# Kernel tuning notes

Hardware: AMD Instinct MI355X
Metric: run time of the kernel (lower is better)

The kernel has to match this reference:

```python
import jax, jax.numpy as jnp
import numpy as np

N = 50000
HID = 128
NH = 4
E_RES, E_SEQ, E_KNN = 100000, 100000, 200000
BN_EPS = 1e-5
NEG_SLOPE = 0.2


def _gat(h, src, dst, W, al, ar, resW, b):
    """DGL-style GATConv (eval mode: feat_drop off, residual=True, bias).
    h: (N, in), W/resW: (in, H*out), al/ar: (H, out), b: (H*out,)"""
    Hh, out = al.shape
    feat = (h @ W).reshape(N, Hh, out)                 # (N, H, out)
    el = jnp.sum(feat * al, axis=-1)                   # (N, H)
    er = jnp.sum(feat * ar, axis=-1)                   # (N, H)
    e = jax.nn.leaky_relu(el[src] + er[dst], NEG_SLOPE)  # (E, H)
    # edge softmax over incoming edges of each dst node (numerically stable)
    m = jax.ops.segment_max(e, dst, num_segments=N)    # (N, H)
    ex = jnp.exp(e - m[dst])
    s = jax.ops.segment_sum(ex, dst, num_segments=N)
    a = ex / s[dst]                                    # (E, H)
    msg = a[:, :, None] * feat[src]                    # (E, H, out)
    rst = jax.ops.segment_sum(msg, dst, num_segments=N)  # (N, H, out)
    return rst + (h @ resW).reshape(N, Hh, out) + b.reshape(1, Hh, out)


def _hetero(h, src_res, dst_res, src_seq, dst_seq, src_knn, dst_knn, W, al, ar, resW, b):
    # HeteroGraphConv with aggregate='sum' over relations, then mean over heads
    r = _gat(h, src_res, dst_res, W[0], al[0], ar[0], resW[0], b[0])
    r = r + _gat(h, src_seq, dst_seq, W[1], al[1], ar[1], resW[1], b[1])
    r = r + _gat(h, src_knn, dst_knn, W[2], al[2], ar[2], resW[2], b[2])
    return jnp.mean(r, axis=1)                         # (N, out)


def setup_inputs() -> dict:
    key = jax.random.key(0)
    ks = iter(jax.random.split(key, 32))
    inp = {}
    inp["x"] = jax.random.normal(next(ks), (N, HID), jnp.float32)
    inp["src_res"] = jax.random.randint(next(ks), (E_RES,), 0, N, jnp.int32)
    inp["dst_res"] = jax.random.randint(next(ks), (E_RES,), 0, N, jnp.int32)
    inp["src_seq"] = jax.random.randint(next(ks), (E_SEQ,), 0, N, jnp.int32)
    inp["dst_seq"] = jax.random.randint(next(ks), (E_SEQ,), 0, N, jnp.int32)
    inp["src_knn"] = jax.random.randint(next(ks), (E_KNN,), 0, N, jnp.int32)
    inp["dst_knn"] = jax.random.randint(next(ks), (E_KNN,), 0, N, jnp.int32)
    sc = 0.05
    for l in (0, 1):
        inp[f"W{l}"] = jax.random.normal(next(ks), (3, HID, NH * HID), jnp.float32) * sc
        inp[f"al{l}"] = jax.random.normal(next(ks), (3, NH, HID), jnp.float32) * sc
        inp[f"ar{l}"] = jax.random.normal(next(ks), (3, NH, HID), jnp.float32) * sc
        inp[f"resW{l}"] = jax.random.normal(next(ks), (3, HID, NH * HID), jnp.float32) * sc
        inp[f"b{l}"] = jax.random.normal(next(ks), (3, NH * HID), jnp.float32) * sc
    inp["fc_W"] = jax.random.normal(next(ks), (HID, HID), jnp.float32) * sc
    inp["fc_b"] = jax.random.normal(next(ks), (HID,), jnp.float32) * sc
    inp["bn_gamma"] = jnp.ones((HID,), jnp.float32)
    inp["bn_beta"] = jnp.zeros((HID,), jnp.float32)
    inp["bn_mean"] = jax.random.normal(next(ks), (HID,), jnp.float32) * sc
    inp["bn_var"] = jax.random.uniform(next(ks), (HID,), jnp.float32)
    return inp


def reference(x, src_res, dst_res, src_seq, dst_seq, src_knn, dst_knn,
              W0, al0, ar0, resW0, b0, W1, al1, ar1, resW1, b1,
              fc_W, fc_b, bn_gamma, bn_beta, bn_mean, bn_var):
    # layer 0: hetero GAT, head-mean, fc + ReLU + BatchNorm (eval), dropout=identity
    h = _hetero(x, src_res, dst_res, src_seq, dst_seq, src_knn, dst_knn,
                W0, al0, ar0, resW0, b0)
    h = jax.nn.relu(h @ fc_W + fc_b)
    h = (h - bn_mean) / jnp.sqrt(bn_var + BN_EPS) * bn_gamma + bn_beta
    # layer 1 (final): hetero GAT, head-mean
    out = _hetero(h, src_res, dst_res, src_seq, dst_seq, src_knn, dst_knn,
                  W1, al1, ar1, resW1, b1)
    return out
```

## Files before the change

### kernel.cpp

```cpp
#include <hip/hip_runtime.h>
#include <hip/hip_bf16.h>
#include <math.h>
#include <stdint.h>

#define NNODES 50000
#define SCHUNK 4096
#define AW 1664
#define XOFF 1536

typedef __bf16 bf16x8 __attribute__((ext_vector_type(8)));
typedef float f32x4 __attribute__((ext_vector_type(4)));
typedef unsigned short u16;
typedef unsigned int u32;

__device__ __forceinline__ float lrelu(float x){ return x >= 0.f ? x : 0.2f*x; }
__device__ __forceinline__ float lo2f(u32 v){ union{ u32 i; float f; } c; c.i = v<<16; return c.f; }
__device__ __forceinline__ float hi2f(u32 v){ union{ u32 i; float f; } c; c.i = v & 0xffff0000u; return c.f; }
__device__ __forceinline__ u16 f2b(float f){ __hip_bfloat16 h = __float2bfloat16(f); return *(u16*)&h; }
__device__ __forceinline__ u32 packbf(float a, float b){ return (u32)f2b(a) | ((u32)f2b(b) << 16); }

#define GLDS16(g, l) __builtin_amdgcn_global_load_lds( \
    (const __attribute__((address_space(1))) void*)(g), \
    (__attribute__((address_space(3))) void*)(l), 16, 0, 0)

__global__ void prep_all(const float* __restrict__ W0, const float* __restrict__ W1,
                         const float* __restrict__ resW0, const float* __restrict__ resW1,
                         const float* __restrict__ b0, const float* __restrict__ b1,
                         const float* __restrict__ al0, const float* __restrict__ ar0,
                         const float* __restrict__ al1, const float* __restrict__ ar1,
                         const float* __restrict__ fcW,
                         u16* __restrict__ Btb, float* __restrict__ biasf,
                         u16* __restrict__ wlb, u16* __restrict__ fcWtb,
                         int* __restrict__ cnt)
{
    int gid = blockIdx.x*blockDim.x + threadIdx.x;
    if (gid < 3*NNODES) cnt[gid] = 0;
    if (gid < 2*128*AW){
        int l = gid / (128*AW);
        int rem = gid - l*(128*AW);
        int c = rem / AW;
        int j = rem - c*AW;
        const float* W  = l ? W1 : W0;
        const float* rw = l ? resW1 : resW0;
        float v;
        if (j < XOFF){
            int r = j >> 9, h = (j >> 7) & 3, k = j & 127;
            v = 0.25f * W[(size_t)r*65536 + (size_t)k*512 + h*128 + c];
        } else {
            int k = j - XOFF;
            float s = 0.f;
            for (int r = 0; r < 3; ++r)
                for (int h = 0; h < 4; ++h)
                    s += rw[(size_t)r*65536 + (size_t)k*512 + h*128 + c];
            v = 0.25f * s;
        }
        Btb[gid] = f2b(v);
    }
    if (gid < 256){
        int l = gid >> 7, c = gid & 127;
        const float* bb = l ? b1 : b0;
        float s = 0.f;
        for (int r = 0; r < 3; ++r)
            for (int h = 0; h < 4; ++h)
                s += bb[r*512 + h*128 + c];
        biasf[gid] = 0.25f*s;
    }
    if (gid < 2*128*128){
        int l = gid >> 14;
        int col = (gid >> 7) & 127;
        int k = gid & 127;
        float v = 0.f;
        if (col < 24){
            int r = col >> 3, lr = (col >> 2) & 1, h = col & 3;
            const float* W = l ? W1 : W0;
            const float* av = l ? (lr ? ar1 : al1) : (lr ? ar0 : al0);
            const float* wrow = W + (size_t)r*65536 + (size_t)k*512 + h*128;
            const float* arow = av + r*512 + h*128;
            for (int cc = 0; cc < 128; ++cc) v += wrow[cc]*arow[cc];
        }
        wlb[gid] = f2b(v);
    }
    if (gid < 128*128){
        int k = gid & 127, n = gid >> 7;
        fcWtb[gid] = f2b(fcW[k*128 + n]);
    }
}

__global__ __launch_bounds__(256) void xprep_kernel(const float* __restrict__ x,
    u16* __restrict__ Ax, const u16* __restrict__ wl, float* __restrict__ el, int M)
{
    __shared__ u16 Xs[64*136];
    __shared__ u16 Ws[32*136];
    const int tid = threadIdx.x;
    const int row0 = blockIdx.x*64;
    #pragma unroll
    for (int p = 0; p < 2; ++p){
        int idx = tid + p*256;
        int c = idx >> 4, kc = (idx & 15)*8;
        float4 v = make_float4(0.f,0.f,0.f,0.f);
        if (c < 24) v = *(const float4*)(wl + c*128 + kc);
        *(float4*)&Ws[c*136 + kc] = v;
    }
    int r = tid >> 2, cq = (tid & 3)*32;
    int grow = row0 + r;
    if (grow < M){
        #pragma unroll
        for (int i = 0; i < 8; ++i){
            float4 v = *(const float4*)(x + (size_t)grow*128 + cq + i*4);
            ushort4 o;
            o.x = f2b(v.x); o.y = f2b(v.y); o.z = f2b(v.z); o.w = f2b(v.w);
            *(ushort4*)(Ax + (size_t)grow*AW + cq + i*4) = o;
            *(ushort4*)&Xs[r*136 + cq + i*4] = o;
        }
    } else {
        ushort4 z; z.x=0; z.y=0; z.z=0; z.w=0;
        #pragma unroll
        for (int i = 0; i < 8; ++i) *(ushort4*)&Xs[r*136 + cq + i*4] = z;
    }
    __syncthreads();
    const int lane = tid & 63, wave = tid >> 6;
    const int r16 = lane & 15, quad = lane >> 4;
    f32x4 acc0 = {}, acc1 = {};
    #pragma unroll
    for (int ks = 0; ks < 4; ++ks){
        int ko = ks*32 + quad*8;
        bf16x8 a  = *(const bf16x8*)&Xs[(wave*16 + r16)*136 + ko];
        bf16x8 b0 = *(const bf16x8*)&Ws[r16*136 + ko];
        bf16x8 b1 = *(const bf16x8*)&Ws[(16 + r16)*136 + ko];
        acc0 = __builtin_amdgcn_mfma_f32_16x16x32_bf16(a, b0, acc0, 0,0,0);
        acc1 = __builtin_amdgcn_mfma_f32_16x16x32_bf16(a, b1, acc1, 0,0,0);
    }
    #pragma unroll
    for (int p = 0; p < 4; ++p){
        int row = row0 + wave*16 + quad*4 + p;
        if (row < M){
            el[(size_t)row*32 + r16] = acc0[p];
            if (r16 < 8) el[(size_t)row*32 + 16 + r16] = acc1[p];
        }
    }
}

__global__ void hist_all(const int* __restrict__ d0, const int* __restrict__ d1,
                         const int* __restrict__ d2, int e0, int e1, int e2,
                         int* __restrict__ cnt)
{
    int g = blockIdx.x*blockDim.x + threadIdx.x;
    if (g >= e0 + e1 + e2) return;
    int rel, idx;
    if (g < e0){ rel = 0; idx = g; }
    else if (g < e0 + e1){ rel = 1; idx = g - e0; }
    else { rel = 2; idx = g - e0 - e1; }
    const int* d = rel == 0 ? d0 : (rel == 1 ? d1 : d2);
    atomicAdd(cnt + (size_t)rel*NNODES + d[idx], 1);
}

__global__ __launch_bounds__(256) void scan_all(const int* __restrict__ cnt_all,
                                                int* __restrict__ rp_all, int* __restrict__ cur_all,
                                                int Nn, int nblk)
{
    int rel = blockIdx.y, blk = blockIdx.x;
    const int* cnt = cnt_all + (size_t)rel*Nn;
    int* rp  = rp_all  + (size_t)rel*(Nn+1);
    int* cur = cur_all + (size_t)rel*Nn;
    int tid = threadIdx.x;
    __shared__ int wsA[4];
    __shared__ int wsum[4];
    __shared__ int sOffS;
    int pre = blk*SCHUNK;
    int s0 = 0;
    for (int i = tid*4; i < pre; i += 1024){
        int4 v = *(const int4*)(cnt + i);
        s0 += v.x + v.y + v.z + v.w;
    }
    #pragma unroll
    for (int off = 1; off < 64; off <<= 1) s0 += __shfl_xor(s0, off);
    if ((tid & 63) == 0) wsA[tid >> 6] = s0;
    __syncthreads();
    if (tid == 0) sOffS = wsA[0] + wsA[1] + wsA[2] + wsA[3];
    int i0 = blk*SCHUNK + tid*16;
    int v[16];
    int s = 0;
    #pragma unroll
    for (int k = 0; k < 16; ++k){
        int idx = i0 + k;
        v[k] = (idx < Nn) ? cnt[idx] : 0;
        s += v[k];
    }
    int lane = tid & 63;
    int incl = s;
    #pragma unroll
    for (int off = 1; off < 64; off <<= 1){
        int t = __shfl_up(incl, off);
        if (lane >= off) incl += t;
    }
    if (lane == 63) wsum[tid >> 6] = incl;
    __syncthreads();
    int sOff = sOffS;
    int woff = 0;
    for (int w = 0; w < (tid >> 6); ++w) woff += wsum[w];
    int ex = sOff + woff + incl - s;
    #pragma unroll
    for (int k = 0; k < 16; ++k){
        int idx = i0 + k;
        if (idx < Nn){ rp[idx] = ex; cur[idx] = ex; }
        ex += v[k];
    }
    if (blk == nblk - 1 && tid == 0)
        rp[Nn] = sOff + wsum[0] + wsum[1] + wsum[2] + wsum[3];
}

__global__ void scatter_all(const int* __restrict__ s0, const int* __restrict__ s1,
                            const int* __restrict__ s2,
                            const int* __restrict__ d0, const int* __restrict__ d1,
                            const int* __restrict__ d2, int e0, int e1, int e2,
                            int* __restrict__ cur, int* __restrict__ colb)
{
    int g = blockIdx.x*blockDim.x + threadIdx.x;
    if (g >= e0 + e1 + e2) return;
    int rel, idx, coff;
    if (g < e0){ rel = 0; idx = g; coff = 0; }
    else if (g < e0 + e1){ rel = 1; idx = g - e0; coff = e0; }
    else { rel = 2; idx = g - e0 - e1; coff = e0 + e1; }
    const int* sp = rel == 0 ? s0 : (rel == 1 ? s1 : s2);
    const int* dp = rel == 0 ? d0 : (rel == 1 ? d1 : d2);
    int d = dp[idx];
    int pos = atomicAdd(cur + (size_t)rel*NNODES + d, 1);
    colb[coff + pos] = sp[idx];
}

__global__ __launch_bounds__(256) void agg3(const int* __restrict__ rowp_all,
    const int* __restrict__ colb_all, int e0, int e01,
    const float* __restrict__ el_all,
    const u16* __restrict__ Ax, u16* __restrict__ Abuf, int Nn)
{
    const int rel = blockIdx.y;
    const int tid = threadIdx.x;
    const int lane = tid & 63;
    const int o = tid & 15;
    const int base = lane & 48;
    const int n = (blockIdx.x*256 + tid) >> 4;
    if (n >= Nn) return;
    const int* rowp = rowp_all + (size_t)rel*(Nn+1);
    const int coff = (rel == 0) ? 0 : ((rel == 1) ? e0 : e01);
    const int* colb = colb_all + coff;
    u16* op = Abuf + (size_t)n*AW + rel*512 + o*8;

    int beg = rowp[n], end = rowp[n+1];
    if (beg >= end){
        uint4 z; z.x = 0; z.y = 0; z.z = 0; z.w = 0;
        #pragma unroll
        for (int h = 0; h < 4; ++h) *(uint4*)(op + h*128) = z;
        return;
    }
    float4 ed = *(const float4*)(el_all + (size_t)n*32 + rel*8 + 4);
    float acc[4][8] = {};
    float us0 = 0.f, us1 = 0.f, us2 = 0.f, us3 = 0.f;

    for (int eb = beg; eb < end; eb += 16){
        int rem = end - eb;
        int cnt16 = rem < 16 ? rem : 16;
        bool val = (o < cnt16);
        int s_l = 0;
        if (val) s_l = colb[eb + o];
        float wl0 = 0.f, wl1 = 0.f, wl2 = 0.f, wl3 = 0.f;
        if (val){
            float4 e_l = *(const float4*)(el_all + (size_t)s_l*32 + rel*8);
            wl0 = __expf(lrelu(e_l.x + ed.x));
            wl1 = __expf(lrelu(e_l.y + ed.y));
            wl2 = __expf(lrelu(e_l.z + ed.z));
            wl3 = __expf(lrelu(e_l.w + ed.w));
        }
        us0 += wl0; us1 += wl1; us2 += wl2; us3 += wl3;
        int st0 = __shfl(s_l, base);
        uint4 xa = *(const uint4*)(Ax + (size_t)st0*AW + o*8);
        uint4 xb = xa;
        if (cnt16 > 1){
            int st1 = __shfl(s_l, base + 1);
            xb = *(const uint4*)(Ax + (size_t)st1*AW + o*8);
        }
        for (int t = 0; t < cnt16; ++t){
            uint4 xc = xb;
            if (t + 2 < cnt16){
                int st2 = __shfl(s_l, base + t + 2);
                xc = *(const uint4*)(Ax + (size_t)st2*AW + o*8);
            }
            float w0 = __shfl(wl0, base + t);
            float w1 = __shfl(wl1, base + t);
            float w2 = __shfl(wl2, base + t);
            float w3 = __shfl(wl3, base + t);
            float xv[8];
            xv[0] = lo2f(xa.x); xv[1] = hi2f(xa.x);
            xv[2] = lo2f(xa.y); xv[3] = hi2f(xa.y);
            xv[4] = lo2f(xa.z); xv[5] = hi2f(xa.z);
            xv[6] = lo2f(xa.w); xv[7] = hi2f(xa.w);
            #pragma unroll
            for (int c = 0; c < 8; ++c){
                acc[0][c] = fmaf(w0, xv[c], acc[0][c]);
                acc[1][c] = fmaf(w1, xv[c], acc[1][c]);
                acc[2][c] = fmaf(w2, xv[c], acc[2][c]);
                acc[3][c] = fmaf(w3, xv[c], acc[3][c]);
            }
            xa = xb; xb = xc;
        }
    }
    #pragma unroll
    for (int off = 1; off < 16; off <<= 1){
        us0 += __shfl_xor(us0, off); us1 += __shfl_xor(us1, off);
        us2 += __shfl_xor(us2, off); us3 += __shfl_xor(us3, off);
    }
    float inv[4] = {1.f/us0, 1.f/us1, 1.f/us2, 1.f/us3};
    #pragma unroll
    for (int h = 0; h < 4; ++h){
        uint4 ov;
        ov.x = packbf(acc[h][0]*inv[h], acc[h][1]*inv[h]);
        ov.y = packbf(acc[h][2]*inv[h], acc[h][3]*inv[h]);
        ov.z = packbf(acc[h][4]*inv[h], acc[h][5]*inv[h]);
        ov.w = packbf(acc[h][6]*inv[h], acc[h][7]*inv[h]);
        *(uint4*)(op + h*128) = ov;
    }
}

template<int EPI, int FCF>
__global__ __launch_bounds__(256, 3) void gemm_f(
    const u16* __restrict__ A, int Astride, int K,
    const u16* __restrict__ Bt,
    float* __restrict__ Cf, u16* __restrict__ Cb, int Cstride, int M,
    const float* __restrict__ bias, const float* __restrict__ gamma,
    const float* __restrict__ beta, const float* __restrict__ mean,
    const float* __restrict__ var,
    const u16* __restrict__ wl, float* __restrict__ el,
    const u16* __restrict__ fcw, const float* __restrict__ fcb2)
{
    __shared__ u16 smem[FCF ? 26112 : 16384];
    const int tid = threadIdx.x;
    const int row0 = blockIdx.x*128;
    const int lane = tid & 63, wave = tid >> 6;
    const int wm = (wave >> 1)*64, wn = (wave & 1)*64;
    const int r16 = lane & 15, quad = lane >> 4;
    const int swzbase = r16 & 7;
    f32x4 acc[4][4] = {};

    const int r8 = lane >> 3, jc = lane & 7;
    const int soff = ((jc ^ r8) << 3);
    const u16* srcA[4];
    const u16* srcB[4];
    #pragma unroll
    for (int g = 0; g < 4; ++g){
        int gr = row0 + wave*32 + g*8 + r8;
        if (gr >= M) gr = M - 1;
        srcA[g] = A + (size_t)gr*Astride + soff;
        srcB[g] = Bt + (size_t)(wave*32 + g*8 + r8)*K + soff;
    }
    u16* As = smem;
    u16* Bs = smem + 8192;
    const int nk = K >> 6;

    for (int t = 0; t < nk; ++t){
        const int k0 = t << 6;
        #pragma unroll
        for (int g = 0; g < 4; ++g){
            GLDS16(srcA[g] + k0, As + wave*2048 + g*512);
            GLDS16(srcB[g] + k0, Bs + wave*2048 + g*512);
        }
        __syncthreads();
        #pragma unroll
        for (int ks = 0; ks < 2; ++ks){
            int swz = ((ks*4 + quad) ^ swzbase) << 3;
            bf16x8 a[4], b[4];
            #pragma unroll
            for (int i = 0; i < 4; ++i) a[i] = *(const bf16x8*)&As[(wm + i*16 + r16)*64 + swz];
            #pragma unroll
            for (int j = 0; j < 4; ++j) b[j] = *(const bf16x8*)&Bs[(wn + j*16 + r16)*64 + swz];
            #pragma unroll
            for (int i = 0; i < 4; ++i)
                #pragma unroll
                for (int j = 0; j < 4; ++j)
                    acc[i][j] = __builtin_amdgcn_mfma_f32_16x16x32_bf16(a[i], b[j], acc[i][j], 0,0,0);
        }
        __syncthreads();
    }

    if (!FCF){
        #pragma unroll
        for (int i = 0; i < 4; ++i){
            #pragma unroll
            for (int p = 0; p < 4; ++p){
                int row = row0 + wm + i*16 + quad*4 + p;
                #pragma unroll
                for (int j = 0; j < 4; ++j){
                    int col = wn + j*16 + r16;
                    float v = acc[i][j][p] + bias[col];
                    if (row < M){
                        if (EPI == 1) Cf[(size_t)row*Cstride + col] = v;
                        else          Cb[(size_t)row*Cstride + col] = f2b(v);
                    }
                }
            }
        }
    } else {
        u16* Cs = smem;
        u16* Ws = smem + 17408;
        #pragma unroll
        for (int i = 0; i < 4; ++i){
            #pragma unroll
            for (int p = 0; p < 4; ++p){
                int rl = wm + i*16 + quad*4 + p;
                #pragma unroll
                for (int j = 0; j < 4; ++j){
                    int col = wn + j*16 + r16;
                    Cs[rl*136 + col] = f2b(acc[i][j][p] + bias[col]);
                }
            }
        }
        __syncthreads();
        f32x4 fa[2][8] = {};
        #pragma unroll
        for (int hh = 0; hh < 2; ++hh){
            {
                int rr = tid >> 2, sg = (tid & 3)*32;
                const u16* src = fcw + (size_t)(hh*64 + rr)*128 + sg;
                #pragma unroll
                for (int q = 0; q < 4; ++q)
                    *(float4*)&Ws[rr*136 + sg + q*8] = *(const float4*)(src + q*8);
            }
            __syncthreads();
            #pragma unroll
            for (int ks = 0; ks < 4; ++ks){
                int ko = ks*32 + quad*8;
                #pragma unroll
                for (int i = 0; i < 2; ++i){
                    bf16x8 a = *(const bf16x8*)&Cs[(wave*32 + i*16 + r16)*136 + ko];
                    #pragma unroll
                    for (int jj = 0; jj < 4; ++jj){
                        bf16x8 b = *(const bf16x8*)&Ws[(jj*16 + r16)*136 + ko];
                        fa[i][hh*4+jj] = __builtin_amdgcn_mfma_f32_16x16x32_bf16(a, b, fa[i][hh*4+jj], 0,0,0);
                    }
                }
            }
            __syncthreads();
        }
        #pragma unroll
        for (int f = 0; f < 8; ++f){
            int col = f*16 + r16;
            float fb = fcb2[col];
            float mn = mean[col];
            float sc = gamma[col]*rsqrtf(var[col] + 1e-5f);
            float bt = beta[col];
            #pragma unroll
            for (int i = 0; i < 2; ++i){
                #pragma unroll
                for (int p = 0; p < 4; ++p){
                    int rl = wave*32 + i*16 + quad*4 + p;
                    int row = row0 + rl;
                    float v = fa[i][f][p] + fb;
                    v = fmaxf(v, 0.f);
                    v = (v - mn)*sc + bt;
                    u16 vb = f2b(v);
                    if (row < M) Cb[(size_t)row*Cstride + col] = vb;
                    Cs[rl*136 + col] = vb;
                }
            }
        }
        #pragma unroll
        for (int p = 0; p < 2; ++p){
            int idx = tid + p*256;
            int c = idx >> 4, kc = (idx & 15)*8;
            float4 v = make_float4(0.f,0.f,0.f,0.f);
            if (c < 24) v = *(const float4*)(wl + c*128 + kc);
            *(float4*)&Ws[c*136 + kc] = v;
        }
        __syncthreads();
        f32x4 e0[2] = {}, e1[2] = {};
        #pragma unroll
        for (int ks = 0; ks < 4; ++ks){
            int ko = ks*32 + quad*8;
            #pragma unroll
            for (int i = 0; i < 2; ++i){
                bf16x8 a  = *(const bf16x8*)&Cs[(wave*32 + i*16 + r16)*136 + ko];
                bf16x8 b0 = *(const bf16x8*)&Ws[r16*136 + ko];
                bf16x8 b1 = *(const bf16x8*)&Ws[(16 + r16)*136 + ko];
                e0[i] = __builtin_amdgcn_mfma_f32_16x16x32_bf16(a, b0, e0[i], 0,0,0);
                e1[i] = __builtin_amdgcn_mfma_f32_16x16x32_bf16(a, b1, e1[i], 0,0,0);
            }
        }
        #pragma unroll
        for (int i = 0; i < 2; ++i){
            #pragma unroll
            for (int p = 0; p < 4; ++p){
                int row = row0 + wave*32 + i*16 + quad*4 + p;
                if (row < M){
                    el[(size_t)row*32 + r16] = e0[i][p];
                    if (r16 < 8) el[(size_t)row*32 + 16 + r16] = e1[i][p];
                }
            }
        }
    }
}

static inline char* align256(char* p){ return (char*)(((uintptr_t)p + 255) & ~(uintptr_t)255); }

extern "C" void kernel_launch(void* const* d_in, const int* in_sizes, int n_in,
                              void* d_out, int out_size, void* d_ws, size_t ws_size,
                              hipStream_t stream)
{
    const float* x      = (const float*)d_in[0];
    const int* srcs[3]  = {(const int*)d_in[1], (const int*)d_in[3], (const int*)d_in[5]};
    const int* dsts[3]  = {(const int*)d_in[2], (const int*)d_in[4], (const int*)d_in[6]};
    const int  E[3]     = {in_sizes[1], in_sizes[3], in_sizes[5]};
    const float* W0     = (const float*)d_in[7];
    const float* al0    = (const float*)d_in[8];
    const float* ar0    = (const float*)d_in[9];
    const float* resW0  = (const float*)d_in[10];
    const float* b0     = (const float*)d_in[11];
    const float* W1     = (const float*)d_in[12];
    const float* al1    = (const float*)d_in[13];
    const float* ar1    = (const float*)d_in[14];
    const float* resW1  = (const float*)d_in[15];
    const float* b1     = (const float*)d_in[16];
    const float* fcW    = (const float*)d_in[17];
    const float* fcb    = (const float*)d_in[18];
    const float* gamma  = (const float*)d_in[19];
    const float* beta   = (const float*)d_in[20];
    const float* bmean  = (const float*)d_in[21];
    const float* bvar   = (const float*)d_in[22];
    float* out = (float*)d_out;

    char* p = (char*)d_ws;
    u16*   Abuf  = (u16*)p;   p += (size_t)NNODES*AW*2;    p = align256(p);
    float* el    = (float*)p; p += (size_t)NNODES*32*4;    p = align256(p);
    int*   cnt   = (int*)p;   p += (size_t)3*NNODES*4;     p = align256(p);
    int*   rowp  = (int*)p;   p += (size_t)3*(NNODES+1)*4; p = align256(p);
    int*   cur   = (int*)p;   p += (size_t)3*NNODES*4;     p = align256(p);
    int*   colb  = (int*)p;   p += (size_t)(E[0]+E[1]+E[2])*4; p = align256(p);
    u16*   Btb   = (u16*)p;   p += (size_t)2*128*AW*2;     p = align256(p);
    u16*   wlb   = (u16*)p;   p += (size_t)2*128*128*2;    p = align256(p);
    u16*   fcWtb = (u16*)p;   p += (size_t)128*128*2;      p = align256(p);
    float* biasf = (float*)p; p += (size_t)2*128*4;        p = align256(p);

    const int NBLK = (NNODES + SCHUNK - 1)/SCHUNK;
    const int MB64 = (NNODES + 63)/64;
    const int MBG  = (NNODES + 127)/128;
    const int AGGBLKS = (NNODES*16 + 255)/256;
    const int ETOT = E[0] + E[1] + E[2];
    dim3 blk(256);
    u16* Ax = Abuf + XOFF;

    prep_all<<<(2*128*AW + 255)/256, blk, 0, stream>>>(W0, W1, resW0, resW1, b0, b1,
                                                       al0, ar0, al1, ar1, fcW,
                                                       Btb, biasf, wlb, fcWtb, cnt);
    xprep_kernel<<<MB64, blk, 0, stream>>>(x, Ax, wlb, el, NNODES);
    hist_all<<<(ETOT + 255)/256, blk, 0, stream>>>(dsts[0], dsts[1], dsts[2], E[0], E[1], E[2], cnt);
    scan_all<<<dim3(NBLK,3), blk, 0, stream>>>(cnt, rowp, cur, NNODES, NBLK);
    scatter_all<<<(ETOT + 255)/256, blk, 0, stream>>>(srcs[0], srcs[1], srcs[2],
                                                      dsts[0], dsts[1], dsts[2],
                                                      E[0], E[1], E[2], cur, colb);

    agg3<<<dim3(AGGBLKS,3), blk, 0, stream>>>(rowp, colb, E[0], E[0]+E[1], el, Ax, Abuf, NNODES);
    gemm_f<0,1><<<MBG, blk, 0, stream>>>(Abuf, AW, AW, Btb, nullptr, Ax, AW, NNODES,
                                         biasf, gamma, beta, bmean, bvar,
                                         wlb + 16384, el, fcWtb, fcb);

    agg3<<<dim3(AGGBLKS,3), blk, 0, stream>>>(rowp, colb, E[0], E[0]+E[1], el, Ax, Abuf, NNODES);
    gemm_f<1,0><<<MBG, blk, 0, stream>>>(Abuf, AW, AW, Btb + (size_t)128*AW, out, nullptr, 128, NNODES,
                                         biasf + 128, nullptr, nullptr, nullptr, nullptr,
                                         nullptr, nullptr, nullptr, nullptr);
}
```

Baseline: 361.0 us.

## Double-buffer GEMM LDS tiles and use packed FP32 FMAs in aggregation

The GEMM main loop now keeps two LDS stages. It issues the global-to-LDS loads for the next K tile before computing on the current one, so load latency overlaps the MFMA work and one barrier per iteration is removed. This doubles the shared memory footprint to 64KB per block, so the launch bound drops from 3 to 2 blocks per CU. Separately, the edge aggregation loop stores its accumulators as float2 vectors so the compiler can emit packed FP32 FMAs, roughly halving the FMA instruction count in that inner loop.

```diff
diff --git a/kernel.cpp b/kernel.cpp
--- a/kernel.cpp
+++ b/kernel.cpp
@@ -10,12 +10,14 @@
 
 typedef __bf16 bf16x8 __attribute__((ext_vector_type(8)));
 typedef float f32x4 __attribute__((ext_vector_type(4)));
+typedef float f32x2 __attribute__((ext_vector_type(2)));
 typedef unsigned short u16;
 typedef unsigned int u32;
 
 __device__ __forceinline__ float lrelu(float x){ return x >= 0.f ? x : 0.2f*x; }
 __device__ __forceinline__ float lo2f(u32 v){ union{ u32 i; float f; } c; c.i = v<<16; return c.f; }
 __device__ __forceinline__ float hi2f(u32 v){ union{ u32 i; float f; } c; c.i = v & 0xffff0000u; return c.f; }
+__device__ __forceinline__ f32x2 up2(u32 v){ f32x2 r; r.x = lo2f(v); r.y = hi2f(v); return r; }
 __device__ __forceinline__ u16 f2b(float f){ __hip_bfloat16 h = __float2bfloat16(f); return *(u16*)&h; }
 __device__ __forceinline__ u32 packbf(float a, float b){ return (u32)f2b(a) | ((u32)f2b(b) << 16); }
 
@@ -253,7 +255,7 @@
         return;
     }
     float4 ed = *(const float4*)(el_all + (size_t)n*32 + rel*8 + 4);
-    float acc[4][8] = {};
+    f32x2 acc2[4][4] = {};
     float us0 = 0.f, us1 = 0.f, us2 = 0.f, us3 = 0.f;
 
     for (int eb = beg; eb < end; eb += 16){
@@ -284,21 +286,19 @@
                 int st2 = __shfl(s_l, base + t + 2);
                 xc = *(const uint4*)(Ax + (size_t)st2*AW + o*8);
             }
-            float w0 = __shfl(wl0, base + t);
-            float w1 = __shfl(wl1, base + t);
-            float w2 = __shfl(wl2, base + t);
-            float w3 = __shfl(wl3, base + t);
-            float xv[8];
-            xv[0] = lo2f(xa.x); xv[1] = hi2f(xa.x);
-            xv[2] = lo2f(xa.y); xv[3] = hi2f(xa.y);
-            xv[4] = lo2f(xa.z); xv[5] = hi2f(xa.z);
-            xv[6] = lo2f(xa.w); xv[7] = hi2f(xa.w);
-            #pragma unroll
-            for (int c = 0; c < 8; ++c){
-                acc[0][c] = fmaf(w0, xv[c], acc[0][c]);
-                acc[1][c] = fmaf(w1, xv[c], acc[1][c]);
-                acc[2][c] = fmaf(w2, xv[c], acc[2][c]);
-                acc[3][c] = fmaf(w3, xv[c], acc[3][c]);
+            f32x2 w0p, w1p, w2p, w3p;
+            { float w = __shfl(wl0, base + t); w0p.x = w; w0p.y = w; }
+            { float w = __shfl(wl1, base + t); w1p.x = w; w1p.y = w; }
+            { float w = __shfl(wl2, base + t); w2p.x = w; w2p.y = w; }
+            { float w = __shfl(wl3, base + t); w3p.x = w; w3p.y = w; }
+            f32x2 xv[4];
+            xv[0] = up2(xa.x); xv[1] = up2(xa.y); xv[2] = up2(xa.z); xv[3] = up2(xa.w);
+            #pragma unroll
+            for (int c = 0; c < 4; ++c){
+                acc2[0][c] += w0p * xv[c];
+                acc2[1][c] += w1p * xv[c];
+                acc2[2][c] += w2p * xv[c];
+                acc2[3][c] += w3p * xv[c];
             }
             xa = xb; xb = xc;
         }
@@ -312,16 +312,16 @@
     #pragma unroll
     for (int h = 0; h < 4; ++h){
         uint4 ov;
-        ov.x = packbf(acc[h][0]*inv[h], acc[h][1]*inv[h]);
-        ov.y = packbf(acc[h][2]*inv[h], acc[h][3]*inv[h]);
-        ov.z = packbf(acc[h][4]*inv[h], acc[h][5]*inv[h]);
-        ov.w = packbf(acc[h][6]*inv[h], acc[h][7]*inv[h]);
+        ov.x = packbf(acc2[h][0].x*inv[h], acc2[h][0].y*inv[h]);
+        ov.y = packbf(acc2[h][1].x*inv[h], acc2[h][1].y*inv[h]);
+        ov.z = packbf(acc2[h][2].x*inv[h], acc2[h][2].y*inv[h]);
+        ov.w = packbf(acc2[h][3].x*inv[h], acc2[h][3].y*inv[h]);
         *(uint4*)(op + h*128) = ov;
     }
 }
 
 template<int EPI, int FCF>
-__global__ __launch_bounds__(256, 3) void gemm_f(
+__global__ __launch_bounds__(256, 2) void gemm_f(
     const u16* __restrict__ A, int Astride, int K,
     const u16* __restrict__ Bt,
     float* __restrict__ Cf, u16* __restrict__ Cb, int Cstride, int M,
@@ -331,7 +331,7 @@
     const u16* __restrict__ wl, float* __restrict__ el,
     const u16* __restrict__ fcw, const float* __restrict__ fcb2)
 {
-    __shared__ u16 smem[FCF ? 26112 : 16384];
+    __shared__ u16 smem[32768];
     const int tid = threadIdx.x;
     const int row0 = blockIdx.x*128;
     const int lane = tid & 63, wave = tid >> 6;
@@ -351,18 +351,25 @@
         srcA[g] = A + (size_t)gr*Astride + soff;
         srcB[g] = Bt + (size_t)(wave*32 + g*8 + r8)*K + soff;
     }
-    u16* As = smem;
-    u16* Bs = smem + 8192;
     const int nk = K >> 6;
 
+    #define STAGE(buf, t) do { \
+        u16* As_ = smem + (buf)*16384; \
+        u16* Bs_ = As_ + 8192; \
+        const int k0_ = (t) << 6; \
+        _Pragma("unroll") \
+        for (int g_ = 0; g_ < 4; ++g_){ \
+            GLDS16(srcA[g_] + k0_, As_ + wave*2048 + g_*512); \
+            GLDS16(srcB[g_] + k0_, Bs_ + wave*2048 + g_*512); \
+        } \
+    } while (0)
+
+    STAGE(0, 0);
+    __syncthreads();
     for (int t = 0; t < nk; ++t){
-        const int k0 = t << 6;
-        #pragma unroll
-        for (int g = 0; g < 4; ++g){
-            GLDS16(srcA[g] + k0, As + wave*2048 + g*512);
-            GLDS16(srcB[g] + k0, Bs + wave*2048 + g*512);
-        }
-        __syncthreads();
+        if (t + 1 < nk) STAGE((t+1)&1, t+1);
+        const u16* As = smem + (t&1)*16384;
+        const u16* Bs = As + 8192;
         #pragma unroll
         for (int ks = 0; ks < 2; ++ks){
             int swz = ((ks*4 + quad) ^ swzbase) << 3;
@@ -379,6 +386,7 @@
         }
         __syncthreads();
     }
+    #undef STAGE
 
     if (!FCF){
         #pragma unroll
```

After: 351.7 us (median of 2 runs). 1.03x faster.
